# Kernel tuning notes

Measured on AMD Instinct MI355X. Metric: run time of the kernel, lower is better.

Reference implementation:

```python
import jax, jax.numpy as jnp
import numpy as np

G, N, D, L, T = 64, 64, 128, 4, 10
SLOPE = 0.01
BN_EPS = 1e-5


def _gin(x, adj, mask, W1, b1, W2, b2, eps):
    # x: [B,N,D], adj: [B,N,N], mask: [B,N] bool
    agg = jnp.einsum('bnm,bmd->bnd', adj, x)
    h = (1.0 + eps) * x + agg
    h = jax.nn.leaky_relu(h @ W1 + b1, SLOPE)
    h = h @ W2 + b2
    return h * mask[..., None].astype(h.dtype)


def _masked_bn(h, mask, gamma, beta):
    # training-mode BatchNorm1d over the masked (valid) rows only
    m = mask[..., None].astype(h.dtype)
    cnt = jnp.sum(m)
    mean = jnp.sum(h * m, axis=(0, 1)) / cnt
    var = jnp.sum(((h - mean) ** 2) * m, axis=(0, 1)) / cnt  # biased, as BN
    hn = (h - mean) * jax.lax.rsqrt(var + BN_EPS) * gamma + beta
    return jnp.where(mask[..., None], hn, h)


def _seg_mean(v, idx, num_segments):
    s = jax.ops.segment_sum(v, idx, num_segments=num_segments)
    c = jax.ops.segment_sum(jnp.ones((v.shape[0],), v.dtype), idx, num_segments=num_segments)
    return s / jnp.maximum(c, 1.0).reshape((num_segments,) + (1,) * (v.ndim - 1))


def setup_inputs() -> dict:
    key = jax.random.key(0)
    ks = jax.random.split(key, 16)
    S = G * N
    # original graphs: symmetric binary adjacency, no self loops
    a = (jax.random.uniform(ks[0], (G, N, N)) > 0.9).astype(jnp.float32)
    a = jnp.triu(a, 1)
    original_adj = a + a.transpose(0, 2, 1)
    original_mask = jnp.ones((G, N), dtype=bool)
    # node-deleted policy: subgraph s of graph s//N deletes node s%N
    graph_idx = jnp.repeat(jnp.arange(G), N)
    deleted = jnp.tile(jnp.arange(N), G)
    mask = jnp.ones((S, N), dtype=bool).at[jnp.arange(S), deleted].set(False)
    mf = mask.astype(jnp.float32)
    adj = original_adj[graph_idx] * mf[:, :, None] * mf[:, None, :]
    x = jax.random.normal(ks[1], (S, N, D), dtype=jnp.float32)
    sc = 1.0 / np.sqrt(D)
    inp = dict(
        x=x, adj=adj, original_adj=original_adj,
        gnn_W1=jax.random.normal(ks[2], (L, D, D)) * sc,
        gnn_b1=jnp.zeros((L, D)),
        gnn_W2=jax.random.normal(ks[3], (L, D, D)) * sc,
        gnn_b2=jnp.zeros((L, D)),
        gnn_eps=jnp.zeros((L,)),
        gs_W1=jax.random.normal(ks[4], (L, D, D)) * sc,
        gs_b1=jnp.zeros((L, D)),
        gs_W2=jax.random.normal(ks[5], (L, D, D)) * sc,
        gs_b2=jnp.zeros((L, D)),
        gs_eps=jnp.zeros((L,)),
        bn_gamma=jnp.ones((L, D)), bn_beta=jnp.zeros((L, D)),
        bns_gamma=jnp.ones((L, D)), bns_beta=jnp.zeros((L, D)),
        fin_W1=jax.random.normal(ks[6], (D, 2 * D)) * sc,
        fin_b1=jnp.zeros((2 * D,)),
        fin_W2=jax.random.normal(ks[7], (2 * D, T)) * (1.0 / np.sqrt(2 * D)),
        fin_b2=jnp.zeros((T,)),
        mask=mask, original_mask=original_mask, graph_idx=graph_idx,
    )
    return inp


def reference(x, adj, original_adj, gnn_W1, gnn_b1, gnn_W2, gnn_b2, gnn_eps,
              gs_W1, gs_b1, gs_W2, gs_b2, gs_eps,
              bn_gamma, bn_beta, bns_gamma, bns_beta,
              fin_W1, fin_b1, fin_W2, fin_b2,
              mask, original_mask, graph_idx):
    for i in range(L):
        h1 = _gin(x, adj, mask, gnn_W1[i], gnn_b1[i], gnn_W2[i], gnn_b2[i], gnn_eps[i])
        h1 = _masked_bn(h1, mask, bn_gamma[i], bn_beta[i])
        x_sum = _seg_mean(x, graph_idx, G)  # [G,N,D] scatter-mean over subgraphs
        h2 = _gin(x_sum, original_adj, original_mask, gs_W1[i], gs_b1[i], gs_W2[i], gs_b2[i], gs_eps[i])
        h2 = _masked_bn(h2, original_mask, bns_gamma[i], bns_beta[i])
        x = jax.nn.leaky_relu(h1 + h2[graph_idx], SLOPE)
    num_nodes = jnp.sum(mask, axis=-1).astype(x.dtype)  # [S]
    h_sub = jnp.sum(x, axis=1) / num_nodes[:, None]     # mean pool per subgraph
    h_graph = _seg_mean(h_sub, graph_idx, G)            # [G,D]
    out = jax.nn.leaky_relu(h_graph @ fin_W1 + fin_b1, SLOPE) @ fin_W2 + fin_b2
    return out
```

## Files before the change

### kernel.cpp

```cpp
#include <hip/hip_runtime.h>
#include <hip/hip_bf16.h>


typedef __bf16 bf16x8 __attribute__((ext_vector_type(8)));
typedef float f32x4 __attribute__((ext_vector_type(4)));
typedef unsigned short us8 __attribute__((ext_vector_type(8)));
typedef unsigned short us4 __attribute__((ext_vector_type(4)));

__device__ __forceinline__ unsigned short f2b(float f) {
  unsigned u = __builtin_bit_cast(unsigned, f);
  u += 0x7FFFu + ((u >> 16) & 1u);
  return (unsigned short)(u >> 16);
}
__device__ __forceinline__ float b2f(unsigned short h) {
  return __builtin_bit_cast(float, (unsigned)h << 16);
}
__device__ __forceinline__ f32x4 mm(bf16x8 a, bf16x8 b, f32x4 c) {
  return __builtin_amdgcn_mfma_f32_16x16x32_bf16(a, b, c, 0, 0, 0);
}
__device__ __forceinline__ bf16x8 frag(const char* base, int row, int Kelems, int k0) {
  int off = (row * Kelems + k0) * 2;
  off ^= (row & 7) << 4;
  return *(const bf16x8*)(base + off);
}
__device__ __forceinline__ float lk(float v) { return v > 0.f ? v : 0.01f * v; }

__global__ __launch_bounds__(256) void k_prep(const float* __restrict__ g1,
    const float* __restrict__ g2, const float* __restrict__ s1,
    const float* __restrict__ s2, unsigned short* __restrict__ wt) {
  int b = blockIdx.x;
  int l = b >> 2, j = b & 3;
  const float* src = (j == 0 ? g1 : j == 1 ? g2 : j == 2 ? s1 : s2) + l * 16384;
  unsigned short* dst = wt + b * 16384;
  for (int e = threadIdx.x; e < 16384; e += 256) {
    int n = e >> 7, k = e & 127;
    dst[e] = f2b(src[k * 128 + n]);
  }
}

__global__ __launch_bounds__(256) void k_pack(const float* __restrict__ src,
                                              unsigned short* __restrict__ dst) {
  int sub = blockIdx.x, t = threadIdx.x;
  const float* p = src + (size_t)sub * 4096 + (t >> 2) * 64 + (t & 3) * 16;
  unsigned bits = 0;
  #pragma unroll
  for (int j4 = 0; j4 < 4; ++j4) {
    float4 v = *(const float4*)(p + j4 * 4);
    bits |= (unsigned)(v.x != 0.f) << (j4 * 4);
    bits |= (unsigned)(v.y != 0.f) << (j4 * 4 + 1);
    bits |= (unsigned)(v.z != 0.f) << (j4 * 4 + 2);
    bits |= (unsigned)(v.w != 0.f) << (j4 * 4 + 3);
  }
  dst[(size_t)sub * 256 + t] = (unsigned short)bits;
}

__global__ __launch_bounds__(256) void k_castseg(const float* __restrict__ x,
    unsigned short* __restrict__ xw, float* __restrict__ pxs) {
  int b2 = blockIdx.x, bb = b2 >> 2, c = b2 & 3, t = threadIdx.x;
  int e0 = c * 2048 + t * 8;
  float acc[8];
  #pragma unroll
  for (int j = 0; j < 8; ++j) acc[j] = 0.f;
  for (int ss = 0; ss < 16; ++ss) {
    size_t sb = ((size_t)bb * 16 + ss) * 8192 + e0;
    float4 v0 = *(const float4*)(x + sb);
    float4 v1 = *(const float4*)(x + sb + 4);
    acc[0] += v0.x; acc[1] += v0.y; acc[2] += v0.z; acc[3] += v0.w;
    acc[4] += v1.x; acc[5] += v1.y; acc[6] += v1.z; acc[7] += v1.w;
    us8 h;
    h[0] = f2b(v0.x); h[1] = f2b(v0.y); h[2] = f2b(v0.z); h[3] = f2b(v0.w);
    h[4] = f2b(v1.x); h[5] = f2b(v1.y); h[6] = f2b(v1.z); h[7] = f2b(v1.w);
    *(us8*)(xw + sb) = h;
  }
  float* o = pxs + (size_t)bb * 8192 + e0;
  *(float4*)o = make_float4(acc[0], acc[1], acc[2], acc[3]);
  *(float4*)(o + 4) = make_float4(acc[4], acc[5], acc[6], acc[7]);
}

__global__ __launch_bounds__(256) void k_h2fix(const unsigned short* __restrict__ h2T,
    const float* __restrict__ bnsA, const float* __restrict__ bnsB,
    float* __restrict__ h2fT) {
  int idx = blockIdx.x * 256 + threadIdx.x;
  int e0 = idx * 16;
  int d = (e0 >> 6) & 127;
  float A2 = bnsA[d], B2 = bnsB[d];
  us8 v0 = *(const us8*)(h2T + e0);
  us8 v1 = *(const us8*)(h2T + e0 + 8);
  float o[16];
  #pragma unroll
  for (int j = 0; j < 8; ++j) { o[j] = fmaf(b2f(v0[j]), A2, B2); o[8 + j] = fmaf(b2f(v1[j]), A2, B2); }
  #pragma unroll
  for (int c = 0; c < 4; ++c)
    *(float4*)(h2fT + e0 + c * 4) = make_float4(o[c * 4], o[c * 4 + 1], o[c * 4 + 2], o[c * 4 + 3]);
}

template<int LAST>
__global__ __launch_bounds__(256) void k_xpart(const unsigned short* __restrict__ h1T,
    const float* __restrict__ h2fT, const float* __restrict__ bnA,
    const float* __restrict__ bnB, float* __restrict__ pxsT,
    float* __restrict__ ppool) {
  int b2 = blockIdx.x, bb = b2 >> 2, c = b2 & 3, g = bb >> 2;
  int t = threadIdx.x;
  int d = c * 32 + (t >> 3), n0 = (t & 7) * 8;
  size_t off = (size_t)d * 64 + n0;
  float A1 = bnA[d], B1 = bnB[d];
  float hb[8];
  *(float4*)hb       = *(const float4*)(h2fT + (size_t)g * 8192 + off);
  *(float4*)(hb + 4) = *(const float4*)(h2fT + (size_t)g * 8192 + off + 4);
  float acc[8];
  #pragma unroll
  for (int j = 0; j < 8; ++j) acc[j] = 0.f;
  for (int ss = 0; ss < 16; ++ss) {
    int s = bb * 16 + ss;
    int del = s & 63;
    us8 a = *(const us8*)(h1T + (size_t)s * 8192 + off);
    #pragma unroll
    for (int j = 0; j < 8; ++j) {
      float hv = ((n0 + j) != del) ? fmaf(b2f(a[j]), A1, B1) : 0.f;
      acc[j] += lk(hv + hb[j]);
    }
  }
  if (!LAST) {
    float* o = pxsT + (size_t)bb * 8192 + off;
    *(float4*)o       = make_float4(acc[0], acc[1], acc[2], acc[3]);
    *(float4*)(o + 4) = make_float4(acc[4], acc[5], acc[6], acc[7]);
  } else {
    float s8 = ((acc[0] + acc[1]) + (acc[2] + acc[3])) + ((acc[4] + acc[5]) + (acc[6] + acc[7]));
    s8 += __shfl_xor(s8, 1, 64);
    s8 += __shfl_xor(s8, 2, 64);
    s8 += __shfl_xor(s8, 4, 64);
    if ((t & 7) == 0) ppool[(size_t)bb * 128 + d] = s8;
  }
}

template<int FIRST>
__global__ __launch_bounds__(512, 4) void k_gin(
    const unsigned short* __restrict__ xw, unsigned short* __restrict__ h1T,
    unsigned short* __restrict__ h2T, const float* __restrict__ h2fT,
    const float* __restrict__ pxs,
    const unsigned short* __restrict__ badj, const unsigned short* __restrict__ boadj,
    const unsigned short* __restrict__ W1g, const unsigned short* __restrict__ W2g,
    const unsigned short* __restrict__ W1s, const unsigned short* __restrict__ W2s,
    const float* __restrict__ b1g, const float* __restrict__ b2g,
    const float* __restrict__ b1s, const float* __restrict__ b2s,
    const float* __restrict__ epg, const float* __restrict__ epss,
    const float* __restrict__ bnA, const float* __restrict__ bnB,
    float* __restrict__ p1s, float* __restrict__ p1q,
    float* __restrict__ p2s, float* __restrict__ p2q) {
  __shared__ __align__(16) char lds[40960];
  char* ldsAdj = lds;
  char* ldsB   = lds + 8192;
  char* ldsC   = lds + 24576;

  const int tid = threadIdx.x;
  const int bid = blockIdx.x;
  const bool SUB = bid < 4096;
  const int lb = SUB ? bid : bid - 4096;
  const int wv = tid >> 6, ln = tid & 63;
  const int lr = ln & 15, lkh = ln >> 4;
  const int wrow = wv * 16 + lr;
  const float ep1 = 1.0f + (SUB ? epg[0] : epss[0]);
  const int del = SUB ? (bid & 63) : -1;
  const unsigned short* W1t = SUB ? W1g : W1s;
  const unsigned short* W2t = SUB ? W2g : W2s;

  bf16x8 w1f[4], w2f[4];
  #pragma unroll
  for (int kk = 0; kk < 4; ++kk) {
    w1f[kk] = *(const bf16x8*)(W1t + (size_t)wrow * 128 + kk * 32 + lkh * 8);
    w2f[kk] = *(const bf16x8*)(W2t + (size_t)wrow * 128 + kk * 32 + lkh * 8);
  }
  const float bb1 = (SUB ? b1g : b1s)[wrow];
  const float bb2 = (SUB ? b2g : b2s)[wrow];

  {
    const unsigned char* bits =
        (const unsigned char*)(SUB ? badj + (size_t)lb * 256 : boadj + (size_t)lb * 256);
    unsigned char bbt = bits[tid];
    int row = tid >> 3, o = tid & 7;
    unsigned short ep1b = f2b(ep1);
    us8 v;
    #pragma unroll
    for (int j = 0; j < 8; ++j) v[j] = ((bbt >> j) & 1) ? (unsigned short)0x3F80 : (unsigned short)0;
    int j0 = row - o * 8;
    if (j0 >= 0 && j0 < 8) v[j0] = ep1b;
    int e = tid * 8;
    *(us8*)(ldsAdj + ((e << 1) ^ ((row & 7) << 4))) = v;
  }
  if (FIRST) {
    if (SUB) {
      const unsigned short* xg = xw + (size_t)bid * 8192;
      for (int e = tid * 8; e < 8192; e += 4096)
        *(us8*)(ldsC + e * 2) = *(const us8*)(xg + e);
    } else {
      const float* p = pxs + (size_t)lb * 4 * 8192;
      int e0 = tid * 16;
      #pragma unroll
      for (int cc = 0; cc < 4; ++cc) {
        float4 s = {0.f, 0.f, 0.f, 0.f};
        #pragma unroll
        for (int qt = 0; qt < 4; ++qt) {
          float4 v = *(const float4*)(p + qt * 8192 + e0 + cc * 4);
          s.x += v.x; s.y += v.y; s.z += v.z; s.w += v.w;
        }
        us4 h; h.x = f2b(s.x * 0.015625f); h.y = f2b(s.y * 0.015625f);
        h.z = f2b(s.z * 0.015625f); h.w = f2b(s.w * 0.015625f);
        *(us4*)(ldsC + (e0 + cc * 4) * 2) = h;
      }
    }
    __syncthreads();
    int d = tid & 127, mg = (tid >> 7) * 16;
    #pragma unroll
    for (int mb = 0; mb < 16; mb += 8) {
      us8 v;
      #pragma unroll
      for (int j = 0; j < 8; ++j)
        v[j] = *(const unsigned short*)(ldsC + ((mg + mb + j) << 8) + (d << 1));
      *(us8*)(ldsB + (((d << 7) + ((mg + mb) << 1)) ^ ((d & 7) << 4))) = v;
    }
  } else {
    int d = tid >> 2, n0 = (tid & 3) * 16;
    if (SUB) {
      const unsigned short* h1g = h1T + (size_t)bid * 8192 + d * 64 + n0;
      const float* h2g = h2fT + (size_t)(bid >> 6) * 8192 + d * 64 + n0;
      float A1 = bnA[d], B1 = bnB[d];
      #pragma unroll
      for (int cc = 0; cc < 2; ++cc) {
        us8 a = *(const us8*)(h1g + cc * 8);
        float hb[8];
        *(float4*)hb       = *(const float4*)(h2g + cc * 8);
        *(float4*)(hb + 4) = *(const float4*)(h2g + cc * 8 + 4);
        us8 o;
        #pragma unroll
        for (int j = 0; j < 8; ++j) {
          int m = n0 + cc * 8 + j;
          float hv = (m != del) ? fmaf(b2f(a[j]), A1, B1) : 0.f;
          o[j] = f2b(lk(hv + hb[j]));
        }
        *(us8*)(ldsB + (((d * 64 + n0 + cc * 8) * 2) ^ ((d & 7) << 4))) = o;
      }
    } else {
      const float* p = pxs + (size_t)lb * 4 * 8192 + d * 64 + n0;
      #pragma unroll
      for (int cc = 0; cc < 4; ++cc) {
        float4 s = {0.f, 0.f, 0.f, 0.f};
        #pragma unroll
        for (int qt = 0; qt < 4; ++qt) {
          float4 v = *(const float4*)(p + qt * 8192 + cc * 4);
          s.x += v.x; s.y += v.y; s.z += v.z; s.w += v.w;
        }
        us4 h; h.x = f2b(s.x * 0.015625f); h.y = f2b(s.y * 0.015625f);
        h.z = f2b(s.z * 0.015625f); h.w = f2b(s.w * 0.015625f);
        *(us4*)(ldsB + (((d * 64 + n0 + cc * 4) * 2) ^ ((d & 7) << 4))) = h;
      }
    }
  }
  __syncthreads();

  {
    f32x4 acc[4] = {};
    #pragma unroll
    for (int rt = 0; rt < 4; ++rt) {
      #pragma unroll
      for (int k0 = 0; k0 < 64; k0 += 32) {
        bf16x8 a = frag(ldsAdj, rt * 16 + lr, 64, k0 + lkh * 8);
        bf16x8 b = frag(ldsB, wrow, 64, k0 + lkh * 8);
        acc[rt] = mm(a, b, acc[rt]);
      }
    }
    #pragma unroll
    for (int rt = 0; rt < 4; ++rt) {
      #pragma unroll
      for (int r = 0; r < 4; ++r) {
        int row = rt * 16 + lkh * 4 + r;
        *(unsigned short*)(ldsC + (((row << 8) + (wrow << 1)) ^ ((row & 7) << 4))) = f2b(acc[rt][r]);
      }
    }
  }
  __syncthreads();

  #pragma unroll
  for (int rt = 0; rt < 4; ++rt) {
    f32x4 acc = {};
    #pragma unroll
    for (int kk = 0; kk < 4; ++kk) {
      bf16x8 a = frag(ldsC, rt * 16 + lr, 128, kk * 32 + lkh * 8);
      acc = mm(a, w1f[kk], acc);
    }
    #pragma unroll
    for (int r = 0; r < 4; ++r) {
      int row = rt * 16 + lkh * 4 + r;
      *(unsigned short*)(ldsB + (((row << 8) + (wrow << 1)) ^ ((row & 7) << 4))) = f2b(lk(acc[r] + bb1));
    }
  }
  __syncthreads();

  {
    float sm = 0.f, sq = 0.f;
    #pragma unroll
    for (int rt = 0; rt < 4; ++rt) {
      f32x4 acc = {};
      #pragma unroll
      for (int kk = 0; kk < 4; ++kk) {
        bf16x8 a = frag(ldsB, rt * 16 + lr, 128, kk * 32 + lkh * 8);
        acc = mm(a, w2f[kk], acc);
      }
      us4 h4;
      #pragma unroll
      for (int r = 0; r < 4; ++r) {
        int m = rt * 16 + lkh * 4 + r;
        float v = acc[r] + bb2;
        if (m == del) v = 0.f;
        sm += v; sq += v * v;
        h4[r] = f2b(v);
      }
      *(us4*)(ldsC + (((wrow * 64 + rt * 16 + lkh * 4) * 2) ^ ((wrow & 7) << 4))) = h4;
    }
    sm += __shfl_xor(sm, 16, 64); sm += __shfl_xor(sm, 32, 64);
    sq += __shfl_xor(sq, 16, 64); sq += __shfl_xor(sq, 32, 64);
    if (ln < 16) {
      float* ps = SUB ? p1s + (size_t)bid * 128 : p2s + (size_t)lb * 128;
      float* pq = SUB ? p1q + (size_t)bid * 128 : p2q + (size_t)lb * 128;
      ps[wrow] = sm;
      pq[wrow] = sq;
    }
  }
  __syncthreads();

  unsigned short* hout = SUB ? h1T + (size_t)bid * 8192 : h2T + (size_t)lb * 8192;
  {
    int e0 = tid * 16;
    int d = e0 >> 6;
    *(us8*)(hout + e0)     = *(const us8*)(ldsC + (((e0)     * 2) ^ ((d & 7) << 4)));
    *(us8*)(hout + e0 + 8) = *(const us8*)(ldsC + (((e0 + 8) * 2) ^ ((d & 7) << 4)));
  }
}

__global__ __launch_bounds__(256) void k_bnred(const float* __restrict__ p1s,
    const float* __restrict__ p1q, float* __restrict__ q1s, float* __restrict__ q1q) {
  __shared__ float red[512];
  int b = blockIdx.x, tid = threadIdx.x;
  int d = tid & 127, jh = tid >> 7;
  float s = 0.f, q = 0.f;
  for (int j = b * 64 + jh; j < b * 64 + 64; j += 2) {
    s += p1s[(size_t)j * 128 + d];
    q += p1q[(size_t)j * 128 + d];
  }
  red[tid] = s; red[256 + tid] = q;
  __syncthreads();
  if (tid < 128) {
    q1s[(size_t)b * 128 + d] = red[d] + red[d + 128];
    q1q[(size_t)b * 128 + d] = red[256 + d] + red[384 + d];
  }
}

__global__ __launch_bounds__(128) void k_bnfin(const float* __restrict__ q1s,
    const float* __restrict__ q1q, const float* __restrict__ p2s,
    const float* __restrict__ p2q, const float* __restrict__ gam1,
    const float* __restrict__ bet1, const float* __restrict__ gam2,
    const float* __restrict__ bet2, float* __restrict__ bnA, float* __restrict__ bnB,
    float* __restrict__ bnsA, float* __restrict__ bnsB) {
  int d = threadIdx.x;
  float s = 0.f, q = 0.f, s2 = 0.f, q2 = 0.f;
  for (int j = 0; j < 64; ++j) {
    s  += q1s[j * 128 + d];  q  += q1q[j * 128 + d];
    s2 += p2s[j * 128 + d];  q2 += p2q[j * 128 + d];
  }
  const float cnt1 = 4096.0f * 63.0f;
  float mean = s / cnt1;
  float var = q / cnt1 - mean * mean;
  float A = gam1[d] * rsqrtf(var + 1e-5f);
  bnA[d] = A; bnB[d] = bet1[d] - mean * A;
  float mean2 = s2 / 4096.0f;
  float var2 = q2 / 4096.0f - mean2 * mean2;
  float A2 = gam2[d] * rsqrtf(var2 + 1e-5f);
  bnsA[d] = A2; bnsB[d] = bet2[d] - mean2 * A2;
}

__global__ __launch_bounds__(256) void k_final(const float* __restrict__ ppool,
    const float* __restrict__ W1, const float* __restrict__ b1,
    const float* __restrict__ W2, const float* __restrict__ b2,
    float* __restrict__ out) {
  __shared__ float hg[128];
  __shared__ float z[256];
  int g = blockIdx.x, t = threadIdx.x;
  if (t < 128) {
    float s = ppool[(size_t)(g * 4 + 0) * 128 + t] + ppool[(size_t)(g * 4 + 1) * 128 + t]
            + ppool[(size_t)(g * 4 + 2) * 128 + t] + ppool[(size_t)(g * 4 + 3) * 128 + t];
    hg[t] = s * (1.0f / (63.0f * 64.0f));
  }
  __syncthreads();
  float a = b1[t];
  for (int d = 0; d < 128; ++d) a = fmaf(hg[d], W1[d * 256 + t], a);
  z[t] = lk(a);
  __syncthreads();
  if (t < 10) {
    float o = b2[t];
    for (int j = 0; j < 256; ++j) o = fmaf(z[j], W2[j * 10 + t], o);
    out[g * 10 + t] = o;
  }
}

extern "C" void kernel_launch(void* const* d_in, const int* in_sizes, int n_in,
                              void* d_out, int out_size, void* d_ws, size_t ws_size,
                              hipStream_t stream) {
  (void)in_sizes; (void)n_in; (void)out_size; (void)ws_size;
  const float* x    = (const float*)d_in[0];
  const float* adj  = (const float*)d_in[1];
  const float* oadj = (const float*)d_in[2];
  const float* gW1  = (const float*)d_in[3];
  const float* gb1  = (const float*)d_in[4];
  const float* gW2  = (const float*)d_in[5];
  const float* gb2  = (const float*)d_in[6];
  const float* geps = (const float*)d_in[7];
  const float* sW1  = (const float*)d_in[8];
  const float* sb1  = (const float*)d_in[9];
  const float* sW2  = (const float*)d_in[10];
  const float* sb2  = (const float*)d_in[11];
  const float* seps = (const float*)d_in[12];
  const float* bng  = (const float*)d_in[13];
  const float* bnb  = (const float*)d_in[14];
  const float* bnsg = (const float*)d_in[15];
  const float* bnsb = (const float*)d_in[16];
  const float* fW1  = (const float*)d_in[17];
  const float* fb1  = (const float*)d_in[18];
  const float* fW2  = (const float*)d_in[19];
  const float* fb2  = (const float*)d_in[20];
  float* out = (float*)d_out;

  char* w = (char*)d_ws;
  unsigned short* xw   = (unsigned short*)w; w += 67108864;
  unsigned short* h1T  = (unsigned short*)w; w += 67108864;
  unsigned short* h2T  = (unsigned short*)w; w += 1048576;
  unsigned short* badj = (unsigned short*)w; w += 2097152;
  unsigned short* boadj= (unsigned short*)w; w += 32768;
  unsigned short* wt   = (unsigned short*)w; w += 524288;
  float* h2fT = (float*)w;          w += 2097152;
  float* pxs  = (float*)w;          w += 8388608;
  float* p1s  = (float*)w;          w += 2097152;
  float* p1q  = (float*)w;          w += 2097152;
  float* p2s  = (float*)w;          w += 32768;
  float* p2q  = (float*)w;          w += 32768;
  float* q1s  = (float*)w;          w += 32768;
  float* q1q  = (float*)w;          w += 32768;
  float* bnA  = (float*)w;          w += 512;
  float* bnB  = (float*)w;          w += 512;
  float* bnsA = (float*)w;          w += 512;
  float* bnsB = (float*)w;          w += 512;
  float* ppool= (float*)w;          w += 131072;

  k_prep<<<16, 256, 0, stream>>>(gW1, gW2, sW1, sW2, wt);
  k_pack<<<4096, 256, 0, stream>>>(adj, badj);
  k_pack<<<64, 256, 0, stream>>>(oadj, boadj);
  k_castseg<<<1024, 256, 0, stream>>>(x, xw, pxs);

  for (int i = 0; i < 4; ++i) {
    if (i > 0)
      k_xpart<0><<<1024, 256, 0, stream>>>(h1T, h2fT, bnA, bnB, pxs, ppool);
    if (i == 0)
      k_gin<1><<<4160, 512, 0, stream>>>(xw, h1T, h2T, h2fT, pxs, badj, boadj,
          wt + 0 * 16384, wt + 1 * 16384, wt + 2 * 16384, wt + 3 * 16384,
          gb1, gb2, sb1, sb2, geps, seps, bnA, bnB, p1s, p1q, p2s, p2q);
    else
      k_gin<0><<<4160, 512, 0, stream>>>(xw, h1T, h2T, h2fT, pxs, badj, boadj,
          wt + (i * 4 + 0) * 16384, wt + (i * 4 + 1) * 16384,
          wt + (i * 4 + 2) * 16384, wt + (i * 4 + 3) * 16384,
          gb1 + i * 128, gb2 + i * 128, sb1 + i * 128, sb2 + i * 128,
          geps + i, seps + i, bnA, bnB, p1s, p1q, p2s, p2q);
    k_bnred<<<64, 256, 0, stream>>>(p1s, p1q, q1s, q1q);
    k_bnfin<<<1, 128, 0, stream>>>(q1s, q1q, p2s, p2q, bng + i * 128,
        bnb + i * 128, bnsg + i * 128, bnsb + i * 128, bnA, bnB, bnsA, bnsB);
    k_h2fix<<<128, 256, 0, stream>>>(h2T, bnsA, bnsB, h2fT);
  }
  k_xpart<1><<<1024, 256, 0, stream>>>(h1T, h2fT, bnA, bnB, pxs, ppool);
  k_final<<<64, 256, 0, stream>>>(ppool, fW1, fb1, fW2, fb2, out);
}
```

Before: 458.8 us.

## Fuse h2 BN-apply into consumers, double-buffer h2, use packed bf16 converts

Drops the k_h2fix kernel. The batchnorm affine for h2 is now applied inside k_xpart and k_gin, which read the bf16 h2 directly instead of a materialised fp32 copy. Because k_gin writes the new h2 while it still reads the previous one, h2 is double-buffered across layers. All scalar bf16 rounding is replaced with the hardware v_cvt_pk_bf16_f32 packed convert, and leaky-relu now uses fmax. The aim is fewer launches, less fp32 traffic and cheaper conversion ALU work, at the cost of a small rounding-mode difference.

```diff
diff --git a/kernel.cpp b/kernel.cpp
--- a/kernel.cpp
+++ b/kernel.cpp
@@ -6,12 +6,19 @@
 typedef float f32x4 __attribute__((ext_vector_type(4)));
 typedef unsigned short us8 __attribute__((ext_vector_type(8)));
 typedef unsigned short us4 __attribute__((ext_vector_type(4)));
+typedef unsigned u32x4 __attribute__((ext_vector_type(4)));
+typedef unsigned u32x2 __attribute__((ext_vector_type(2)));
 
 __device__ __forceinline__ unsigned short f2b(float f) {
   unsigned u = __builtin_bit_cast(unsigned, f);
   u += 0x7FFFu + ((u >> 16) & 1u);
   return (unsigned short)(u >> 16);
 }
+__device__ __forceinline__ unsigned cvtpk(float lo, float hi) {
+  unsigned r;
+  asm("v_cvt_pk_bf16_f32 %0, %1, %2" : "=v"(r) : "v"(lo), "v"(hi));
+  return r;
+}
 __device__ __forceinline__ float b2f(unsigned short h) {
   return __builtin_bit_cast(float, (unsigned)h << 16);
 }
@@ -23,7 +30,7 @@
   off ^= (row & 7) << 4;
   return *(const bf16x8*)(base + off);
 }
-__device__ __forceinline__ float lk(float v) { return v > 0.f ? v : 0.01f * v; }
+__device__ __forceinline__ float lk(float v) { return fmaxf(v, 0.01f * v); }
 
 __global__ __launch_bounds__(256) void k_prep(const float* __restrict__ g1,
     const float* __restrict__ g2, const float* __restrict__ s1,
@@ -67,46 +74,34 @@
     float4 v1 = *(const float4*)(x + sb + 4);
     acc[0] += v0.x; acc[1] += v0.y; acc[2] += v0.z; acc[3] += v0.w;
     acc[4] += v1.x; acc[5] += v1.y; acc[6] += v1.z; acc[7] += v1.w;
-    us8 h;
-    h[0] = f2b(v0.x); h[1] = f2b(v0.y); h[2] = f2b(v0.z); h[3] = f2b(v0.w);
-    h[4] = f2b(v1.x); h[5] = f2b(v1.y); h[6] = f2b(v1.z); h[7] = f2b(v1.w);
-    *(us8*)(xw + sb) = h;
+    u32x4 pk;
+    pk.x = cvtpk(v0.x, v0.y); pk.y = cvtpk(v0.z, v0.w);
+    pk.z = cvtpk(v1.x, v1.y); pk.w = cvtpk(v1.z, v1.w);
+    *(us8*)(xw + sb) = __builtin_bit_cast(us8, pk);
   }
   float* o = pxs + (size_t)bb * 8192 + e0;
   *(float4*)o = make_float4(acc[0], acc[1], acc[2], acc[3]);
   *(float4*)(o + 4) = make_float4(acc[4], acc[5], acc[6], acc[7]);
 }
 
-__global__ __launch_bounds__(256) void k_h2fix(const unsigned short* __restrict__ h2T,
-    const float* __restrict__ bnsA, const float* __restrict__ bnsB,
-    float* __restrict__ h2fT) {
-  int idx = blockIdx.x * 256 + threadIdx.x;
-  int e0 = idx * 16;
-  int d = (e0 >> 6) & 127;
-  float A2 = bnsA[d], B2 = bnsB[d];
-  us8 v0 = *(const us8*)(h2T + e0);
-  us8 v1 = *(const us8*)(h2T + e0 + 8);
-  float o[16];
-  #pragma unroll
-  for (int j = 0; j < 8; ++j) { o[j] = fmaf(b2f(v0[j]), A2, B2); o[8 + j] = fmaf(b2f(v1[j]), A2, B2); }
-  #pragma unroll
-  for (int c = 0; c < 4; ++c)
-    *(float4*)(h2fT + e0 + c * 4) = make_float4(o[c * 4], o[c * 4 + 1], o[c * 4 + 2], o[c * 4 + 3]);
-}
-
 template<int LAST>
 __global__ __launch_bounds__(256) void k_xpart(const unsigned short* __restrict__ h1T,
-    const float* __restrict__ h2fT, const float* __restrict__ bnA,
-    const float* __restrict__ bnB, float* __restrict__ pxsT,
+    const unsigned short* __restrict__ h2T, const float* __restrict__ bnA,
+    const float* __restrict__ bnB, const float* __restrict__ bnsA,
+    const float* __restrict__ bnsB, float* __restrict__ pxsT,
     float* __restrict__ ppool) {
   int b2 = blockIdx.x, bb = b2 >> 2, c = b2 & 3, g = bb >> 2;
   int t = threadIdx.x;
   int d = c * 32 + (t >> 3), n0 = (t & 7) * 8;
   size_t off = (size_t)d * 64 + n0;
   float A1 = bnA[d], B1 = bnB[d];
+  float A2 = bnsA[d], B2 = bnsB[d];
   float hb[8];
-  *(float4*)hb       = *(const float4*)(h2fT + (size_t)g * 8192 + off);
-  *(float4*)(hb + 4) = *(const float4*)(h2fT + (size_t)g * 8192 + off + 4);
+  {
+    us8 v = *(const us8*)(h2T + (size_t)g * 8192 + off);
+    #pragma unroll
+    for (int j = 0; j < 8; ++j) hb[j] = fmaf(b2f(v[j]), A2, B2);
+  }
   float acc[8];
   #pragma unroll
   for (int j = 0; j < 8; ++j) acc[j] = 0.f;
@@ -136,7 +131,7 @@
 template<int FIRST>
 __global__ __launch_bounds__(512, 4) void k_gin(
     const unsigned short* __restrict__ xw, unsigned short* __restrict__ h1T,
-    unsigned short* __restrict__ h2T, const float* __restrict__ h2fT,
+    const unsigned short* __restrict__ h2prev, unsigned short* __restrict__ h2out,
     const float* __restrict__ pxs,
     const unsigned short* __restrict__ badj, const unsigned short* __restrict__ boadj,
     const unsigned short* __restrict__ W1g, const unsigned short* __restrict__ W2g,
@@ -145,6 +140,7 @@
     const float* __restrict__ b1s, const float* __restrict__ b2s,
     const float* __restrict__ epg, const float* __restrict__ epss,
     const float* __restrict__ bnA, const float* __restrict__ bnB,
+    const float* __restrict__ bnsA, const float* __restrict__ bnsB,
     float* __restrict__ p1s, float* __restrict__ p1q,
     float* __restrict__ p2s, float* __restrict__ p2q) {
   __shared__ __align__(16) char lds[40960];
@@ -203,9 +199,10 @@
           float4 v = *(const float4*)(p + qt * 8192 + e0 + cc * 4);
           s.x += v.x; s.y += v.y; s.z += v.z; s.w += v.w;
         }
-        us4 h; h.x = f2b(s.x * 0.015625f); h.y = f2b(s.y * 0.015625f);
-        h.z = f2b(s.z * 0.015625f); h.w = f2b(s.w * 0.015625f);
-        *(us4*)(ldsC + (e0 + cc * 4) * 2) = h;
+        u32x2 pk;
+        pk.x = cvtpk(s.x * 0.015625f, s.y * 0.015625f);
+        pk.y = cvtpk(s.z * 0.015625f, s.w * 0.015625f);
+        *(us4*)(ldsC + (e0 + cc * 4) * 2) = __builtin_bit_cast(us4, pk);
       }
     }
     __syncthreads();
@@ -222,22 +219,24 @@
     int d = tid >> 2, n0 = (tid & 3) * 16;
     if (SUB) {
       const unsigned short* h1g = h1T + (size_t)bid * 8192 + d * 64 + n0;
-      const float* h2g = h2fT + (size_t)(bid >> 6) * 8192 + d * 64 + n0;
+      const unsigned short* h2g = h2prev + (size_t)(bid >> 6) * 8192 + d * 64 + n0;
       float A1 = bnA[d], B1 = bnB[d];
+      float A2 = bnsA[d], B2 = bnsB[d];
       #pragma unroll
       for (int cc = 0; cc < 2; ++cc) {
         us8 a = *(const us8*)(h1g + cc * 8);
-        float hb[8];
-        *(float4*)hb       = *(const float4*)(h2g + cc * 8);
-        *(float4*)(hb + 4) = *(const float4*)(h2g + cc * 8 + 4);
-        us8 o;
+        us8 b = *(const us8*)(h2g + cc * 8);
+        float xv[8];
         #pragma unroll
         for (int j = 0; j < 8; ++j) {
           int m = n0 + cc * 8 + j;
           float hv = (m != del) ? fmaf(b2f(a[j]), A1, B1) : 0.f;
-          o[j] = f2b(lk(hv + hb[j]));
+          xv[j] = lk(hv + fmaf(b2f(b[j]), A2, B2));
         }
-        *(us8*)(ldsB + (((d * 64 + n0 + cc * 8) * 2) ^ ((d & 7) << 4))) = o;
+        u32x4 pk;
+        pk.x = cvtpk(xv[0], xv[1]); pk.y = cvtpk(xv[2], xv[3]);
+        pk.z = cvtpk(xv[4], xv[5]); pk.w = cvtpk(xv[6], xv[7]);
+        *(us8*)(ldsB + (((d * 64 + n0 + cc * 8) * 2) ^ ((d & 7) << 4))) = __builtin_bit_cast(us8, pk);
       }
     } else {
       const float* p = pxs + (size_t)lb * 4 * 8192 + d * 64 + n0;
@@ -249,9 +248,10 @@
           float4 v = *(const float4*)(p + qt * 8192 + cc * 4);
           s.x += v.x; s.y += v.y; s.z += v.z; s.w += v.w;
         }
-        us4 h; h.x = f2b(s.x * 0.015625f); h.y = f2b(s.y * 0.015625f);
-        h.z = f2b(s.z * 0.015625f); h.w = f2b(s.w * 0.015625f);
-        *(us4*)(ldsB + (((d * 64 + n0 + cc * 4) * 2) ^ ((d & 7) << 4))) = h;
+        u32x2 pk;
+        pk.x = cvtpk(s.x * 0.015625f, s.y * 0.015625f);
+        pk.y = cvtpk(s.z * 0.015625f, s.w * 0.015625f);
+        *(us4*)(ldsB + (((d * 64 + n0 + cc * 4) * 2) ^ ((d & 7) << 4))) = __builtin_bit_cast(us4, pk);
       }
     }
   }
@@ -270,11 +270,13 @@
     }
     #pragma unroll
     for (int rt = 0; rt < 4; ++rt) {
-      #pragma unroll
-      for (int r = 0; r < 4; ++r) {
-        int row = rt * 16 + lkh * 4 + r;
-        *(unsigned short*)(ldsC + (((row << 8) + (wrow << 1)) ^ ((row & 7) << 4))) = f2b(acc[rt][r]);
-      }
+      unsigned p01 = cvtpk(acc[rt][0], acc[rt][1]);
+      unsigned p23 = cvtpk(acc[rt][2], acc[rt][3]);
+      int r0 = rt * 16 + lkh * 4;
+      *(unsigned short*)(ldsC + ((((r0 + 0) << 8) + (wrow << 1)) ^ (((r0 + 0) & 7) << 4))) = (unsigned short)p01;
+      *(unsigned short*)(ldsC + ((((r0 + 1) << 8) + (wrow << 1)) ^ (((r0 + 1) & 7) << 4))) = (unsigned short)(p01 >> 16);
+      *(unsigned short*)(ldsC + ((((r0 + 2) << 8) + (wrow << 1)) ^ (((r0 + 2) & 7) << 4))) = (unsigned short)p23;
+      *(unsigned short*)(ldsC + ((((r0 + 3) << 8) + (wrow << 1)) ^ (((r0 + 3) & 7) << 4))) = (unsigned short)(p23 >> 16);
     }
   }
   __syncthreads();
@@ -287,11 +289,15 @@
       bf16x8 a = frag(ldsC, rt * 16 + lr, 128, kk * 32 + lkh * 8);
       acc = mm(a, w1f[kk], acc);
     }
-    #pragma unroll
-    for (int r = 0; r < 4; ++r) {
-      int row = rt * 16 + lkh * 4 + r;
-      *(unsigned short*)(ldsB + (((row << 8) + (wrow << 1)) ^ ((row & 7) << 4))) = f2b(lk(acc[r] + bb1));
-    }
+    float u0 = lk(acc[0] + bb1), u1 = lk(acc[1] + bb1);
+    float u2 = lk(acc[2] + bb1), u3 = lk(acc[3] + bb1);
+    unsigned p01 = cvtpk(u0, u1);
+    unsigned p23 = cvtpk(u2, u3);
+    int r0 = rt * 16 + lkh * 4;
+    *(unsigned short*)(ldsB + ((((r0 + 0) << 8) + (wrow << 1)) ^ (((r0 + 0) & 7) << 4))) = (unsigned short)p01;
+    *(unsigned short*)(ldsB + ((((r0 + 1) << 8) + (wrow << 1)) ^ (((r0 + 1) & 7) << 4))) = (unsigned short)(p01 >> 16);
+    *(unsigned short*)(ldsB + ((((r0 + 2) << 8) + (wrow << 1)) ^ (((r0 + 2) & 7) << 4))) = (unsigned short)p23;
+    *(unsigned short*)(ldsB + ((((r0 + 3) << 8) + (wrow << 1)) ^ (((r0 + 3) & 7) << 4))) = (unsigned short)(p23 >> 16);
   }
   __syncthreads();
 
@@ -305,16 +311,18 @@
         bf16x8 a = frag(ldsB, rt * 16 + lr, 128, kk * 32 + lkh * 8);
         acc = mm(a, w2f[kk], acc);
       }
-      us4 h4;
-      #pragma unroll
-      for (int r = 0; r < 4; ++r) {
-        int m = rt * 16 + lkh * 4 + r;
-        float v = acc[r] + bb2;
-        if (m == del) v = 0.f;
-        sm += v; sq += v * v;
-        h4[r] = f2b(v);
-      }
-      *(us4*)(ldsC + (((wrow * 64 + rt * 16 + lkh * 4) * 2) ^ ((wrow & 7) << 4))) = h4;
+      float v0 = acc[0] + bb2, v1 = acc[1] + bb2, v2 = acc[2] + bb2, v3 = acc[3] + bb2;
+      int m0 = rt * 16 + lkh * 4;
+      if (m0 + 0 == del) v0 = 0.f;
+      if (m0 + 1 == del) v1 = 0.f;
+      if (m0 + 2 == del) v2 = 0.f;
+      if (m0 + 3 == del) v3 = 0.f;
+      sm += v0 + v1 + v2 + v3;
+      sq += v0 * v0 + v1 * v1 + v2 * v2 + v3 * v3;
+      u32x2 pk;
+      pk.x = cvtpk(v0, v1);
+      pk.y = cvtpk(v2, v3);
+      *(us4*)(ldsC + (((wrow * 64 + m0) * 2) ^ ((wrow & 7) << 4))) = __builtin_bit_cast(us4, pk);
     }
     sm += __shfl_xor(sm, 16, 64); sm += __shfl_xor(sm, 32, 64);
     sq += __shfl_xor(sq, 16, 64); sq += __shfl_xor(sq, 32, 64);
@@ -327,7 +335,7 @@
   }
   __syncthreads();
 
-  unsigned short* hout = SUB ? h1T + (size_t)bid * 8192 : h2T + (size_t)lb * 8192;
+  unsigned short* hout = SUB ? h1T + (size_t)bid * 8192 : h2out + (size_t)lb * 8192;
   {
     int e0 = tid * 16;
     int d = e0 >> 6;
@@ -431,11 +439,11 @@
   char* w = (char*)d_ws;
   unsigned short* xw   = (unsigned short*)w; w += 67108864;
   unsigned short* h1T  = (unsigned short*)w; w += 67108864;
-  unsigned short* h2T  = (unsigned short*)w; w += 1048576;
+  unsigned short* h2a  = (unsigned short*)w; w += 1048576;
+  unsigned short* h2b  = (unsigned short*)w; w += 1048576;
   unsigned short* badj = (unsigned short*)w; w += 2097152;
   unsigned short* boadj= (unsigned short*)w; w += 32768;
   unsigned short* wt   = (unsigned short*)w; w += 524288;
-  float* h2fT = (float*)w;          w += 2097152;
   float* pxs  = (float*)w;          w += 8388608;
   float* p1s  = (float*)w;          w += 2097152;
   float* p1q  = (float*)w;          w += 2097152;
@@ -449,29 +457,32 @@
   float* bnsB = (float*)w;          w += 512;
   float* ppool= (float*)w;          w += 131072;
 
+  unsigned short* h2buf[2] = {h2a, h2b};
+
   k_prep<<<16, 256, 0, stream>>>(gW1, gW2, sW1, sW2, wt);
   k_pack<<<4096, 256, 0, stream>>>(adj, badj);
   k_pack<<<64, 256, 0, stream>>>(oadj, boadj);
   k_castseg<<<1024, 256, 0, stream>>>(x, xw, pxs);
 
   for (int i = 0; i < 4; ++i) {
+    unsigned short* h2prev = h2buf[(i + 1) & 1];
+    unsigned short* h2cur  = h2buf[i & 1];
     if (i > 0)
-      k_xpart<0><<<1024, 256, 0, stream>>>(h1T, h2fT, bnA, bnB, pxs, ppool);
+      k_xpart<0><<<1024, 256, 0, stream>>>(h1T, h2prev, bnA, bnB, bnsA, bnsB, pxs, ppool);
     if (i == 0)
-      k_gin<1><<<4160, 512, 0, stream>>>(xw, h1T, h2T, h2fT, pxs, badj, boadj,
+      k_gin<1><<<4160, 512, 0, stream>>>(xw, h1T, h2prev, h2cur, pxs, badj, boadj,
           wt + 0 * 16384, wt + 1 * 16384, wt + 2 * 16384, wt + 3 * 16384,
-          gb1, gb2, sb1, sb2, geps, seps, bnA, bnB, p1s, p1q, p2s, p2q);
+          gb1, gb2, sb1, sb2, geps, seps, bnA, bnB, bnsA, bnsB, p1s, p1q, p2s, p2q);
     else
-      k_gin<0><<<4160, 512, 0, stream>>>(xw, h1T, h2T, h2fT, pxs, badj, boadj,
+      k_gin<0><<<4160, 512, 0, stream>>>(xw, h1T, h2prev, h2cur, pxs, badj, boadj,
           wt + (i * 4 + 0) * 16384, wt + (i * 4 + 1) * 16384,
           wt + (i * 4 + 2) * 16384, wt + (i * 4 + 3) * 16384,
           gb1 + i * 128, gb2 + i * 128, sb1 + i * 128, sb2 + i * 128,
-          geps + i, seps + i, bnA, bnB, p1s, p1q, p2s, p2q);
+          geps + i, seps + i, bnA, bnB, bnsA, bnsB, p1s, p1q, p2s, p2q);
     k_bnred<<<64, 256, 0, stream>>>(p1s, p1q, q1s, q1q);
     k_bnfin<<<1, 128, 0, stream>>>(q1s, q1q, p2s, p2q, bng + i * 128,
         bnb + i * 128, bnsg + i * 128, bnsb + i * 128, bnA, bnB, bnsA, bnsB);
-    k_h2fix<<<128, 256, 0, stream>>>(h2T, bnsA, bnsB, h2fT);
-  }
-  k_xpart<1><<<1024, 256, 0, stream>>>(h1T, h2fT, bnA, bnB, pxs, ppool);
+  }
+  k_xpart<1><<<1024, 256, 0, stream>>>(h1T, h2buf[1], bnA, bnB, bnsA, bnsB, pxs, ppool);
   k_final<<<64, 256, 0, stream>>>(ppool, fW1, fb1, fW2, fb2, out);
 }
```

New measurement: 422.4 us. -7.9%, faster.
